# Performance work log

Measured on AMD Instinct MI355X. Metric: run time of the kernel, lower is better.

## Reference

```python
import jax, jax.numpy as jnp
import numpy as np

# Dims: B=batch, C=in_ch (channels), L=pooled length, N=num_classes
B, C, L, N = 256, 2048, 512, 1000
FINAL_SHIFT = 4            # final_shift init arg
FC_SHIFT = 11              # int(log2(in_ch)) = int(log2(2048))


def dead_shift(x_i32, shift):
    # zero out values with |x| < 2^shift, then arithmetic right shift
    thr = jnp.int32(1 << shift)
    x = jnp.where(jnp.abs(x_i32) >= thr, x_i32, jnp.int32(0))
    return x >> shift  # numpy-style arithmetic shift for signed int32


def shift_clamp_i32_to_i8(x_i32, shift):
    x = dead_shift(x_i32, shift)
    return jnp.clip(x, -128, 127).astype(jnp.int8)


def setup_inputs() -> dict:
    key = jax.random.key(0)
    k1, k2 = jax.random.split(key)
    x = jax.random.randint(k1, (B, C, L), -128, 128, dtype=jnp.int32).astype(jnp.int8)
    weights = jax.random.randint(k2, (N, C), -128, 128, dtype=jnp.int32).astype(jnp.int8)
    return {"x": x, "weights": weights}


def reference(x, weights):
    # sum-pool over L: (B, C, L) -> (B, C) in int32
    acc = jnp.sum(x.astype(jnp.int32), axis=2)
    acc = dead_shift(acc, FINAL_SHIFT)
    # IntLinear: int32 matmul (same math as the torch broadcast-multiply-sum,
    # without materializing the (B, N, C) intermediate)
    w32 = weights.astype(jnp.int32)
    y = jnp.einsum('bc,nc->bn', acc, w32)  # (B, N) int32
    return shift_clamp_i32_to_i8(y, FC_SHIFT)
```

## Files before the change

### kernel.cpp

```cpp
#include <hip/hip_runtime.h>

#define BB 256
#define CC 2048
#define LL 512
#define NN 1000
#define FINAL_SHIFT 4
#define FC_SHIFT 11

#define TBB 64
#define TNN 128
#define BK 64
#define AP 76
#define WP 132

__device__ __forceinline__ int dead_shift_i(int x, int shift) {
    int thr = 1 << shift;
    int ax = x < 0 ? -x : x;
    x = (ax >= thr) ? x : 0;
    return x >> shift;
}

__global__ __launch_bounds__(256) void pool_kernel(const int* __restrict__ x,
                                                   int* __restrict__ acc) {
    int wave = threadIdx.x >> 6;
    int lane = threadIdx.x & 63;
    int g = lane >> 4;
    int j = lane & 15;
    long long rowBase = ((long long)blockIdx.x * 4 + wave) * 8;
    const int* pA = x + (rowBase + g) * (long long)LL;
    const int* pB = x + (rowBase + 4 + g) * (long long)LL;

    int4 v[8], u[8];
#pragma unroll
    for (int c = 0; c < 8; ++c) v[c] = *(const int4*)(pA + c * 64 + j * 4);
#pragma unroll
    for (int c = 0; c < 8; ++c) u[c] = *(const int4*)(pB + c * 64 + j * 4);

    int sA = 0, sB = 0;
#pragma unroll
    for (int c = 0; c < 8; ++c) sA += v[c].x + v[c].y + v[c].z + v[c].w;
#pragma unroll
    for (int c = 0; c < 8; ++c) sB += u[c].x + u[c].y + u[c].z + u[c].w;

    sA += __shfl_xor(sA, 1, 64);  sB += __shfl_xor(sB, 1, 64);
    sA += __shfl_xor(sA, 2, 64);  sB += __shfl_xor(sB, 2, 64);
    sA += __shfl_xor(sA, 4, 64);  sB += __shfl_xor(sB, 4, 64);
    sA += __shfl_xor(sA, 8, 64);  sB += __shfl_xor(sB, 8, 64);

    if (j == 0) {
        acc[rowBase + g]     = dead_shift_i(sA, FINAL_SHIFT);
        acc[rowBase + 4 + g] = dead_shift_i(sB, FINAL_SHIFT);
    }
}

__global__ __launch_bounds__(256) void gemm_kernel(const int* __restrict__ acc,
                                                   const int* __restrict__ w,
                                                   int* __restrict__ partial,
                                                   int kch) {
    __shared__ int As[TBB][AP];
    __shared__ int Ws[BK][WP];

    int b0 = blockIdx.x * TBB;
    int n0 = blockIdx.y * TNN;
    int kbase = blockIdx.z * kch;

    int t  = threadIdx.x;
    int tx = t & 15;
    int ty = t >> 4;

    int r[4][8];
#pragma unroll
    for (int bi = 0; bi < 4; ++bi)
#pragma unroll
        for (int j = 0; j < 8; ++j) r[bi][j] = 0;

    for (int k0 = kbase; k0 < kbase + kch; k0 += BK) {
        {
            int b  = t >> 2;
            int kq = (t & 3) * 16;
            const int* src = acc + (long long)(b0 + b) * CC + k0 + kq;
            int4 u0 = *(const int4*)(src + 0);
            int4 u1 = *(const int4*)(src + 4);
            int4 u2 = *(const int4*)(src + 8);
            int4 u3 = *(const int4*)(src + 12);
            *(int4*)&As[b][kq + 0]  = u0;
            *(int4*)&As[b][kq + 4]  = u1;
            *(int4*)&As[b][kq + 8]  = u2;
            *(int4*)&As[b][kq + 12] = u3;
        }
        {
            int kk = tx * 4;
            int sw = ((tx >> 1) & 3) << 2;
#pragma unroll
            for (int rep = 0; rep < 8; ++rep) {
                int n  = rep * 16 + ty;
                int nn = n0 + n;
                int4 uw = make_int4(0, 0, 0, 0);
                if (nn < NN) uw = *(const int4*)(w + (long long)nn * CC + k0 + kk);
                int c = n ^ sw;
                Ws[kk + 0][c] = uw.x;
                Ws[kk + 1][c] = uw.y;
                Ws[kk + 2][c] = uw.z;
                Ws[kk + 3][c] = uw.w;
            }
        }
        __syncthreads();

#pragma unroll
        for (int kk4 = 0; kk4 < BK; kk4 += 4) {
            int4 a[4];
#pragma unroll
            for (int bi = 0; bi < 4; ++bi)
                a[bi] = *(const int4*)&As[ty * 4 + bi][kk4];
#pragma unroll
            for (int uu = 0; uu < 4; ++uu) {
                int kk  = kk4 + uu;
                int swr = ((kk >> 3) & 3) << 2;
                int c0  = (tx * 4) ^ swr;
                int4 w0 = *(const int4*)&Ws[kk][c0];
                int4 w1 = *(const int4*)&Ws[kk][64 + c0];
#pragma unroll
                for (int bi = 0; bi < 4; ++bi) {
                    int av = (uu == 0) ? a[bi].x : (uu == 1) ? a[bi].y
                           : (uu == 2) ? a[bi].z : a[bi].w;
                    r[bi][0] += __mul24(av, w0.x);
                    r[bi][1] += __mul24(av, w0.y);
                    r[bi][2] += __mul24(av, w0.z);
                    r[bi][3] += __mul24(av, w0.w);
                    r[bi][4] += __mul24(av, w1.x);
                    r[bi][5] += __mul24(av, w1.y);
                    r[bi][6] += __mul24(av, w1.z);
                    r[bi][7] += __mul24(av, w1.w);
                }
            }
        }
        __syncthreads();
    }

    long long base = (long long)blockIdx.z * BB * NN;
#pragma unroll
    for (int bi = 0; bi < 4; ++bi) {
        int b = b0 + ty * 4 + bi;
#pragma unroll
        for (int j = 0; j < 8; ++j) {
            int n = n0 + ((j < 4) ? (tx * 4 + j) : (64 + tx * 4 + (j - 4)));
            if (n < NN)
                partial[base + (long long)b * NN + n] = r[bi][j];
        }
    }
}

__global__ __launch_bounds__(256) void epilogue_kernel(const int* __restrict__ partial,
                                                       int* __restrict__ out, int z) {
    int idx = blockIdx.x * 256 + threadIdx.x;
    if (idx >= BB * NN) return;
    int s = 0;
    for (int i = 0; i < z; ++i) s += partial[(long long)i * BB * NN + idx];
    int v = dead_shift_i(s, FC_SHIFT);
    v = min(127, max(-128, v));
    out[idx] = v;
}

extern "C" void kernel_launch(void* const* d_in, const int* in_sizes, int n_in,
                              void* d_out, int out_size, void* d_ws, size_t ws_size,
                              hipStream_t stream) {
    const int* x = (const int*)d_in[0];
    const int* w = (const int*)d_in[1];
    int* out = (int*)d_out;

    int* acc     = (int*)d_ws;
    int* partial = acc + (size_t)BB * CC;

    size_t accBytes = (size_t)BB * CC * 4;
    int Z = 16;
    while (Z > 1 && ws_size < accBytes + (size_t)Z * BB * NN * 4) Z >>= 1;
    int kch = CC / Z;

    pool_kernel<<<(BB * CC) / 32, 256, 0, stream>>>(x, acc);

    dim3 g2(BB / TBB, (NN + TNN - 1) / TNN, Z);
    gemm_kernel<<<g2, 256, 0, stream>>>(acc, w, partial, kch);

    epilogue_kernel<<<(BB * NN + 255) / 256, 256, 0, stream>>>(partial, out, Z);
}
```

Baseline: 232.7 us.

## Use packed int8 sdot4 with hi/lo split of pooled activations in GEMM

The GEMM packs weights into int8 lanes and splits each pooled activation into a signed high part (x>>6) and an unsigned 6-bit low part, each fitting in int8. Four MACs then run per sdot4 instruction, with the two partial sums recombined as (hi<<6)+lo. This cuts ALU work and shared-memory traffic compared with per-element mul24. The split-K factor drops from 16 to 8, which shrinks the partial buffer and the epilogue reduction but gives fewer blocks for parallelism.

```diff
diff --git a/kernel.cpp b/kernel.cpp
--- a/kernel.cpp
+++ b/kernel.cpp
@@ -10,14 +10,41 @@
 #define TBB 64
 #define TNN 128
 #define BK 64
-#define AP 76
-#define WP 132
+#define NKQ 16
+#define ASTR 36
+#define WSTR 132
+
+#if __has_builtin(__builtin_amdgcn_sdot4)
+#define DOT4(a, b, c) __builtin_amdgcn_sdot4((a), (b), (c), false)
+#else
+static __device__ __forceinline__ int dot4_fb(int a, int b, int c) {
+#pragma unroll
+    for (int j = 0; j < 4; ++j) {
+        int av = (a << (24 - 8 * j)) >> 24;
+        int bv = (b << (24 - 8 * j)) >> 24;
+        c += av * bv;
+    }
+    return c;
+}
+#define DOT4(a, b, c) dot4_fb((a), (b), (c))
+#endif
 
 __device__ __forceinline__ int dead_shift_i(int x, int shift) {
     int thr = 1 << shift;
     int ax = x < 0 ? -x : x;
     x = (ax >= thr) ? x : 0;
     return x >> shift;
+}
+
+__device__ __forceinline__ int pack_hi(int4 u) {
+    return ((u.x >> 6) & 255) | (((u.y >> 6) & 255) << 8) |
+           (((u.z >> 6) & 255) << 16) | (((u.w >> 6) & 255) << 24);
+}
+__device__ __forceinline__ int pack_lo(int4 u) {
+    return (u.x & 63) | ((u.y & 63) << 8) | ((u.z & 63) << 16) | ((u.w & 63) << 24);
+}
+__device__ __forceinline__ int pack_b(int4 u) {
+    return (u.x & 255) | ((u.y & 255) << 8) | ((u.z & 255) << 16) | ((u.w & 255) << 24);
 }
 
 __global__ __launch_bounds__(256) void pool_kernel(const int* __restrict__ x,
@@ -57,80 +84,83 @@
                                                    const int* __restrict__ w,
                                                    int* __restrict__ partial,
                                                    int kch) {
-    __shared__ int As[TBB][AP];
-    __shared__ int Ws[BK][WP];
+    __shared__ int As[TBB][ASTR];
+    __shared__ int Ws[NKQ][WSTR];
 
     int b0 = blockIdx.x * TBB;
     int n0 = blockIdx.y * TNN;
     int kbase = blockIdx.z * kch;
 
-    int t  = threadIdx.x;
-    int tx = t & 15;
-    int ty = t >> 4;
-
-    int r[4][8];
+    int t   = threadIdx.x;
+    int tx4 = (t & 15) * 4;
+    int ty4 = (t >> 4) * 4;
+
+    int rH[4][8], rL[4][8];
 #pragma unroll
     for (int bi = 0; bi < 4; ++bi)
 #pragma unroll
-        for (int j = 0; j < 8; ++j) r[bi][j] = 0;
+        for (int j = 0; j < 8; ++j) { rH[bi][j] = 0; rL[bi][j] = 0; }
 
     for (int k0 = kbase; k0 < kbase + kch; k0 += BK) {
         {
-            int b  = t >> 2;
-            int kq = (t & 3) * 16;
-            const int* src = acc + (long long)(b0 + b) * CC + k0 + kq;
+            int b   = t >> 2;
+            int kq0 = (t & 3) * 4;
+            const int* src = acc + (long long)(b0 + b) * CC + k0 + kq0 * 4;
             int4 u0 = *(const int4*)(src + 0);
             int4 u1 = *(const int4*)(src + 4);
             int4 u2 = *(const int4*)(src + 8);
             int4 u3 = *(const int4*)(src + 12);
-            *(int4*)&As[b][kq + 0]  = u0;
-            *(int4*)&As[b][kq + 4]  = u1;
-            *(int4*)&As[b][kq + 8]  = u2;
-            *(int4*)&As[b][kq + 12] = u3;
+            *(int4*)&As[b][kq0]      = make_int4(pack_hi(u0), pack_hi(u1), pack_hi(u2), pack_hi(u3));
+            *(int4*)&As[b][16 + kq0] = make_int4(pack_lo(u0), pack_lo(u1), pack_lo(u2), pack_lo(u3));
         }
         {
-            int kk = tx * 4;
-            int sw = ((tx >> 1) & 3) << 2;
+            int jq = t & 15;
+            int ng = t >> 4;
 #pragma unroll
             for (int rep = 0; rep < 8; ++rep) {
-                int n  = rep * 16 + ty;
+                int n  = rep * 16 + ng;
                 int nn = n0 + n;
-                int4 uw = make_int4(0, 0, 0, 0);
-                if (nn < NN) uw = *(const int4*)(w + (long long)nn * CC + k0 + kk);
-                int c = n ^ sw;
-                Ws[kk + 0][c] = uw.x;
-                Ws[kk + 1][c] = uw.y;
-                Ws[kk + 2][c] = uw.z;
-                Ws[kk + 3][c] = uw.w;
+                int4 u = make_int4(0, 0, 0, 0);
+                if (nn < NN) u = *(const int4*)(w + (long long)nn * CC + k0 + jq * 4);
+                Ws[jq][n] = pack_b(u);
             }
         }
         __syncthreads();
 
 #pragma unroll
-        for (int kk4 = 0; kk4 < BK; kk4 += 4) {
-            int4 a[4];
-#pragma unroll
-            for (int bi = 0; bi < 4; ++bi)
-                a[bi] = *(const int4*)&As[ty * 4 + bi][kk4];
-#pragma unroll
-            for (int uu = 0; uu < 4; ++uu) {
-                int kk  = kk4 + uu;
-                int swr = ((kk >> 3) & 3) << 2;
-                int c0  = (tx * 4) ^ swr;
-                int4 w0 = *(const int4*)&Ws[kk][c0];
-                int4 w1 = *(const int4*)&Ws[kk][64 + c0];
+        for (int q4 = 0; q4 < NKQ; q4 += 4) {
+            int4 aH[4], aL[4];
+#pragma unroll
+            for (int bi = 0; bi < 4; ++bi) {
+                aH[bi] = *(const int4*)&As[ty4 + bi][q4];
+                aL[bi] = *(const int4*)&As[ty4 + bi][16 + q4];
+            }
+#pragma unroll
+            for (int q = 0; q < 4; ++q) {
+                int4 w0 = *(const int4*)&Ws[q4 + q][tx4];
+                int4 w1 = *(const int4*)&Ws[q4 + q][64 + tx4];
 #pragma unroll
                 for (int bi = 0; bi < 4; ++bi) {
-                    int av = (uu == 0) ? a[bi].x : (uu == 1) ? a[bi].y
-                           : (uu == 2) ? a[bi].z : a[bi].w;
-                    r[bi][0] += __mul24(av, w0.x);
-                    r[bi][1] += __mul24(av, w0.y);
-                    r[bi][2] += __mul24(av, w0.z);
-                    r[bi][3] += __mul24(av, w0.w);
-                    r[bi][4] += __mul24(av, w1.x);
-                    r[bi][5] += __mul24(av, w1.y);
-                    r[bi][6] += __mul24(av, w1.z);
-                    r[bi][7] += __mul24(av, w1.w);
+                    int ah = (q == 0) ? aH[bi].x : (q == 1) ? aH[bi].y
+                           : (q == 2) ? aH[bi].z : aH[bi].w;
+                    int al = (q == 0) ? aL[bi].x : (q == 1) ? aL[bi].y
+                           : (q == 2) ? aL[bi].z : aL[bi].w;
+                    rH[bi][0] = DOT4(ah, w0.x, rH[bi][0]);
+                    rH[bi][1] = DOT4(ah, w0.y, rH[bi][1]);
+                    rH[bi][2] = DOT4(ah, w0.z, rH[bi][2]);
+                    rH[bi][3] = DOT4(ah, w0.w, rH[bi][3]);
+                    rH[bi][4] = DOT4(ah, w1.x, rH[bi][4]);
+                    rH[bi][5] = DOT4(ah, w1.y, rH[bi][5]);
+                    rH[bi][6] = DOT4(ah, w1.z, rH[bi][6]);
+                    rH[bi][7] = DOT4(ah, w1.w, rH[bi][7]);
+                    rL[bi][0] = DOT4(al, w0.x, rL[bi][0]);
+                    rL[bi][1] = DOT4(al, w0.y, rL[bi][1]);
+                    rL[bi][2] = DOT4(al, w0.z, rL[bi][2]);
+                    rL[bi][3] = DOT4(al, w0.w, rL[bi][3]);
+                    rL[bi][4] = DOT4(al, w1.x, rL[bi][4]);
+                    rL[bi][5] = DOT4(al, w1.y, rL[bi][5]);
+                    rL[bi][6] = DOT4(al, w1.z, rL[bi][6]);
+                    rL[bi][7] = DOT4(al, w1.w, rL[bi][7]);
                 }
             }
         }
@@ -140,12 +170,12 @@
     long long base = (long long)blockIdx.z * BB * NN;
 #pragma unroll
     for (int bi = 0; bi < 4; ++bi) {
-        int b = b0 + ty * 4 + bi;
+        int b = b0 + ty4 + bi;
 #pragma unroll
         for (int j = 0; j < 8; ++j) {
-            int n = n0 + ((j < 4) ? (tx * 4 + j) : (64 + tx * 4 + (j - 4)));
+            int n = n0 + ((j < 4) ? (tx4 + j) : (64 + tx4 + (j - 4)));
             if (n < NN)
-                partial[base + (long long)b * NN + n] = r[bi][j];
+                partial[base + (long long)b * NN + n] = (rH[bi][j] << 6) + rL[bi][j];
         }
     }
 }
@@ -172,7 +202,7 @@
     int* partial = acc + (size_t)BB * CC;
 
     size_t accBytes = (size_t)BB * CC * 4;
-    int Z = 16;
+    int Z = 8;
     while (Z > 1 && ws_size < accBytes + (size_t)Z * BB * NN * 4) Z >>= 1;
     int kch = CC / Z;
 
```

New measurement: 226.6 us. -2.6%, faster.
